# Kernel optimization log

Measured on AMD Instinct MI355X. Metric: run time of the kernel, lower is better.

Reference implementation:

```python
import jax, jax.numpy as jnp
import numpy as np

PH, PW = 7, 7          # pooled output size (fixed by offset shape in module)
SPP = 2                # sample_per_part: bilinear samples per bin edge
SS = 0.0625            # spatial_scale = 1/16
TRANS_STD = 0.1


def setup_inputs() -> dict:
    key = jax.random.key(0)
    k1, k2, k3, k4, k5 = jax.random.split(key, 5)
    B, C, H, W = 8, 256, 168, 168
    N = 512
    img = W / SS  # input-image extent = 2688
    features = jax.random.normal(k1, (B, C, H, W), dtype=jnp.float32)
    bidx = jax.random.randint(k2, (N,), 0, B).astype(jnp.float32)
    xs = jnp.sort(jax.random.uniform(k3, (N, 2), minval=0.0, maxval=img - 1.0), axis=1)
    ys = jnp.sort(jax.random.uniform(k4, (N, 2), minval=0.0, maxval=img - 1.0), axis=1)
    rois = jnp.stack([bidx, xs[:, 0], ys[:, 0],
                      jnp.minimum(xs[:, 1] + 16.0, img - 1.0),
                      jnp.minimum(ys[:, 1] + 16.0, img - 1.0)], axis=1)
    offset = jax.random.normal(k5, (N, 2, PH, PW), dtype=jnp.float32)
    return {"features": features, "rois": rois, "offset": offset}


def _deform_roi_pool(features, rois, offset):
    B, C, H, W = features.shape
    off = offset * TRANS_STD  # module scales offsets by trans_std
    bidx = jax.lax.stop_gradient(rois[:, 0]).astype(jnp.int32)
    x1, y1, x2, y2 = rois[:, 1], rois[:, 2], rois[:, 3], rois[:, 4]
    # DCN kernel ROI geometry (0.5-pixel aligned, min size 0.1)
    sw = x1 * SS - 0.5
    sh = y1 * SS - 0.5
    rw = jnp.maximum((x2 + 1.0) * SS - 0.5 - sw, 0.1)
    rh = jnp.maximum((y2 + 1.0) * SS - 0.5 - sh, 0.1)
    bin_w, bin_h = rw / PW, rh / PH
    sub_w, sub_h = bin_w / SPP, bin_h / SPP

    e5 = lambda v: v[:, None, None, None, None]  # [N] -> [N,1,1,1,1]
    pw = jnp.arange(PW, dtype=features.dtype).reshape(1, 1, PW, 1, 1)
    ph = jnp.arange(PH, dtype=features.dtype).reshape(1, PH, 1, 1, 1)
    iw = (jnp.arange(SPP, dtype=features.dtype) + 0.5).reshape(1, 1, 1, 1, SPP)
    ih = (jnp.arange(SPP, dtype=features.dtype) + 0.5).reshape(1, 1, 1, SPP, 1)
    offx = off[:, 0][:, :, :, None, None]  # [N,PH,PW,1,1]
    offy = off[:, 1][:, :, :, None, None]

    # sample coords [N,PH,PW,SPP,SPP]: bin start + per-bin learned shift + sub-sample
    x = e5(sw) + pw * e5(bin_w) + offx * e5(rw) + iw * e5(sub_w)
    y = e5(sh) + ph * e5(bin_h) + offy * e5(rh) + ih * e5(sub_h)

    valid = (x > -0.5) & (x < W - 0.5) & (y > -0.5) & (y < H - 0.5)
    xc = jnp.clip(x, 0.0, W - 1.0)
    yc = jnp.clip(y, 0.0, H - 1.0)
    x0f, y0f = jnp.floor(xc), jnp.floor(yc)
    lx, ly = xc - x0f, yc - y0f
    x0 = x0f.astype(jnp.int32)
    y0 = y0f.astype(jnp.int32)
    x1i = jnp.minimum(x0 + 1, W - 1)
    y1i = jnp.minimum(y0 + 1, H - 1)

    # flat gather over (batch, h, w), channels vectorized
    featf = jnp.transpose(features, (0, 2, 3, 1)).reshape(B * H * W, C)
    base = e5(bidx) * (H * W)
    g = lambda yy, xx: featf[base + yy * W + xx]  # [N,PH,PW,SPP,SPP,C]

    w00 = ((1 - ly) * (1 - lx))[..., None]
    w01 = ((1 - ly) * lx)[..., None]
    w10 = (ly * (1 - lx))[..., None]
    w11 = (ly * lx)[..., None]
    val = w00 * g(y0, x0) + w01 * g(y0, x1i) + w10 * g(y1i, x0) + w11 * g(y1i, x1i)
    val = jnp.where(valid[..., None], val, 0.0)

    s = val.sum(axis=(3, 4))                                   # [N,PH,PW,C]
    cnt = valid.sum(axis=(3, 4)).astype(features.dtype)[..., None]
    out = jnp.where(cnt > 0, s / jnp.maximum(cnt, 1.0), 0.0)
    return jnp.transpose(out, (0, 3, 1, 2))                    # [N,C,PH,PW]


def reference(features, rois, offset):
    return _deform_roi_pool(features, rois, offset)
```

## Files before the change

### kernel.cpp

```cpp
#include <hip/hip_runtime.h>
#include <hip/hip_fp16.h>


#define PH_ 7
#define PW_ 7
#define SPP_ 2
#define SS_ 0.0625f
#define TRANS_STD_ 0.1f
#define B_ 8
#define C_ 256
#define H_ 168
#define W_ 168
#define N_ 512
#define HW_ (H_ * W_)
#define HW4_ (HW_ / 4)
#define BLK_ 512
#define RPC_ 10

__global__ __launch_bounds__(512) void build_roi_lists(
    const float* __restrict__ rois, int* __restrict__ ws)
{
    const int r = threadIdx.x;
    if (r < B_) ws[r] = 0;
    __syncthreads();
    const int b = (int)rois[r * 5 + 0];
    const int pos = atomicAdd(&ws[b], 1);
    ws[B_ + b * N_ + pos] = r;
}

__global__ __launch_bounds__(BLK_) void droi_pool_lds(
    const float* __restrict__ features,
    const float* __restrict__ rois,
    const float* __restrict__ offset,
    float* __restrict__ out,
    const int* __restrict__ ws)
{
    __shared__ __half plane[HW_];

    const int c   = blockIdx.x;
    const int b   = blockIdx.y;
    const int tid = threadIdx.x;

    const float4* __restrict__ f4 =
        reinterpret_cast<const float4*>(features + (size_t)(b * C_ + c) * HW_);
    {
        const int full = HW4_ / BLK_;
#pragma unroll 4
        for (int k = 0; k < full; ++k) {
            const int i = tid + k * BLK_;
            const float4 v = f4[i];
            union { __half2 h[2]; float2 f2; } u;
            u.h[0].x = __float2half(v.x); u.h[0].y = __float2half(v.y);
            u.h[1].x = __float2half(v.z); u.h[1].y = __float2half(v.w);
            *reinterpret_cast<float2*>(&plane[i * 4]) = u.f2;
        }
        const int i = tid + full * BLK_;
        if (i < HW4_) {
            const float4 v = f4[i];
            union { __half2 h[2]; float2 f2; } u;
            u.h[0].x = __float2half(v.x); u.h[0].y = __float2half(v.y);
            u.h[1].x = __float2half(v.z); u.h[1].y = __float2half(v.w);
            *reinterpret_cast<float2*>(&plane[i * 4]) = u.f2;
        }
    }
    __syncthreads();

    const int cnt_b = ws[b];
    const int* __restrict__ list = ws + B_ + b * N_;

    const int q   = tid / 49;
    const int bin = tid - q * 49;
    const int ph  = bin / PW_;
    const int pw  = bin - ph * PW_;
    const bool lane_ok = (q < RPC_);

    for (int base = 0; base < cnt_b; base += RPC_) {
        const int idx     = base + q;
        const bool active = lane_ok && (idx < cnt_b);
        const int r = list[active ? idx : 0];

        const float x1r = rois[r * 5 + 1];
        const float y1r = rois[r * 5 + 2];
        const float x2r = rois[r * 5 + 3];
        const float y2r = rois[r * 5 + 4];

        const float sw    = x1r * SS_ - 0.5f;
        const float sh    = y1r * SS_ - 0.5f;
        const float rw    = fmaxf((x2r + 1.0f) * SS_ - 0.5f - sw, 0.1f);
        const float rh    = fmaxf((y2r + 1.0f) * SS_ - 0.5f - sh, 0.1f);
        const float bin_w = rw * (1.0f / PW_);
        const float bin_h = rh * (1.0f / PH_);
        const float sub_w = bin_w * (1.0f / SPP_);
        const float sub_h = bin_h * (1.0f / SPP_);

        const float offx = offset[((r * 2 + 0) * PH_ + ph) * PW_ + pw] * TRANS_STD_;
        const float offy = offset[((r * 2 + 1) * PH_ + ph) * PW_ + pw] * TRANS_STD_;

        const float bx = sw + (float)pw * bin_w + offx * rw;
        const float by = sh + (float)ph * bin_h + offy * rh;

        float s = 0.0f;
        int cnt = 0;
#pragma unroll
        for (int ihs = 0; ihs < SPP_; ++ihs) {
#pragma unroll
            for (int iws = 0; iws < SPP_; ++iws) {
                const float x = bx + ((float)iws + 0.5f) * sub_w;
                const float y = by + ((float)ihs + 0.5f) * sub_h;
                const bool valid = (x > -0.5f) && (x < (float)W_ - 0.5f) &&
                                   (y > -0.5f) && (y < (float)H_ - 0.5f);
                const float xc = fminf(fmaxf(x, 0.0f), (float)(W_ - 1));
                const float yc = fminf(fmaxf(y, 0.0f), (float)(H_ - 1));
                const float x0f = floorf(xc);
                const float y0f = floorf(yc);
                const float lx = xc - x0f;
                const float ly = yc - y0f;
                const int x0 = (int)x0f;
                const int y0 = (int)y0f;
                const int x1i = min(x0 + 1, W_ - 1);
                const int y1i = min(y0 + 1, H_ - 1);

                const float f00 = __half2float(plane[y0  * W_ + x0 ]);
                const float f01 = __half2float(plane[y0  * W_ + x1i]);
                const float f10 = __half2float(plane[y1i * W_ + x0 ]);
                const float f11 = __half2float(plane[y1i * W_ + x1i]);

                const float v = (1.0f - ly) * (1.0f - lx) * f00 +
                                (1.0f - ly) * lx          * f01 +
                                ly          * (1.0f - lx) * f10 +
                                ly          * lx          * f11;
                if (valid) { s += v; cnt += 1; }
            }
        }

        if (active) {
            const float res = (cnt > 0) ? (s / (float)cnt) : 0.0f;
            out[((size_t)r * C_ + c) * (PH_ * PW_) + bin] = res;
        }
    }
}

__global__ __launch_bounds__(64) void droi_pool_fallback(
    const float* __restrict__ features,
    const float* __restrict__ rois,
    const float* __restrict__ offset,
    float* __restrict__ out)
{
    const int blk  = blockIdx.x;
    const int n    = blk >> 8;
    const int c    = blk & 255;
    const int lane = threadIdx.x;
    if (lane >= PH_ * PW_) return;
    const int ph = lane / PW_;
    const int pw = lane % PW_;

    const float r0  = rois[n * 5 + 0];
    const float x1r = rois[n * 5 + 1];
    const float y1r = rois[n * 5 + 2];
    const float x2r = rois[n * 5 + 3];
    const float y2r = rois[n * 5 + 4];
    const int   b   = (int)r0;

    const float sw    = x1r * SS_ - 0.5f;
    const float sh    = y1r * SS_ - 0.5f;
    const float rw    = fmaxf((x2r + 1.0f) * SS_ - 0.5f - sw, 0.1f);
    const float rh    = fmaxf((y2r + 1.0f) * SS_ - 0.5f - sh, 0.1f);
    const float bin_w = rw / PW_;
    const float bin_h = rh / PH_;
    const float sub_w = bin_w / SPP_;
    const float sub_h = bin_h / SPP_;

    const float offx = offset[((n * 2 + 0) * PH_ + ph) * PW_ + pw] * TRANS_STD_;
    const float offy = offset[((n * 2 + 1) * PH_ + ph) * PW_ + pw] * TRANS_STD_;

    const float bx = sw + (float)pw * bin_w + offx * rw;
    const float by = sh + (float)ph * bin_h + offy * rh;

    const float* __restrict__ f =
        features + (size_t)(b * C_ + c) * (size_t)HW_;

    float s = 0.0f;
    int cnt = 0;
#pragma unroll
    for (int ihs = 0; ihs < SPP_; ++ihs) {
#pragma unroll
        for (int iws = 0; iws < SPP_; ++iws) {
            const float x = bx + ((float)iws + 0.5f) * sub_w;
            const float y = by + ((float)ihs + 0.5f) * sub_h;
            const bool valid = (x > -0.5f) && (x < (float)W_ - 0.5f) &&
                               (y > -0.5f) && (y < (float)H_ - 0.5f);
            const float xc = fminf(fmaxf(x, 0.0f), (float)(W_ - 1));
            const float yc = fminf(fmaxf(y, 0.0f), (float)(H_ - 1));
            const float x0f = floorf(xc);
            const float y0f = floorf(yc);
            const float lx = xc - x0f;
            const float ly = yc - y0f;
            const int x0 = (int)x0f;
            const int y0 = (int)y0f;
            const int x1i = min(x0 + 1, W_ - 1);
            const int y1i = min(y0 + 1, H_ - 1);
            const float f00 = f[y0  * W_ + x0 ];
            const float f01 = f[y0  * W_ + x1i];
            const float f10 = f[y1i * W_ + x0 ];
            const float f11 = f[y1i * W_ + x1i];
            const float v = (1.0f - ly) * (1.0f - lx) * f00 +
                            (1.0f - ly) * lx          * f01 +
                            ly          * (1.0f - lx) * f10 +
                            ly          * lx          * f11;
            if (valid) { s += v; cnt += 1; }
        }
    }
    const float res = (cnt > 0) ? (s / (float)cnt) : 0.0f;
    out[(size_t)(n * C_ + c) * (PH_ * PW_) + lane] = res;
}

extern "C" void kernel_launch(void* const* d_in, const int* in_sizes, int n_in,
                              void* d_out, int out_size, void* d_ws, size_t ws_size,
                              hipStream_t stream) {
    const float* features = (const float*)d_in[0];
    const float* rois     = (const float*)d_in[1];
    const float* offset   = (const float*)d_in[2];
    float*       out      = (float*)d_out;

    const size_t ws_needed = (size_t)(B_ + B_ * N_) * sizeof(int);
    if (ws_size >= ws_needed) {
        int* ws = (int*)d_ws;
        hipLaunchKernelGGL(build_roi_lists, dim3(1), dim3(N_), 0, stream,
                           rois, ws);
        hipLaunchKernelGGL(droi_pool_lds, dim3(C_, B_), dim3(BLK_), 0, stream,
                           features, rois, offset, out, ws);
    } else {
        hipLaunchKernelGGL(droi_pool_fallback, dim3(N_ * C_), dim3(64), 0, stream,
                           features, rois, offset, out);
    }
}
```

Before: 357.4 us.

## Precompute per-ROI sample descriptors and enlarge pooling blocks to 1024 threads

Adds a kernel that computes, once per ROI, bin and sub-sample each packed corner address, interpolation fractions and a validity-scaled weight. This removes the per-channel repetition of the geometry math in the pooling kernel, which now only reads a float4 descriptor and does the interpolation with lerps. The pooling block grows to 1024 threads and handles 20 ROIs per iteration. The trade-off is an extra kernel launch, a larger workspace requirement (about 1.6 MB of descriptors read by every block) and a larger block that may affect occupancy.

```diff
diff --git a/kernel.cpp b/kernel.cpp
--- a/kernel.cpp
+++ b/kernel.cpp
@@ -14,8 +14,15 @@
 #define N_ 512
 #define HW_ (H_ * W_)
 #define HW4_ (HW_ / 4)
-#define BLK_ 512
-#define RPC_ 10
+#define BINS_ (PH_ * PW_)
+#define NSUB_ (SPP_ * SPP_)
+#define BLK_ 1024
+#define RPC_ 20
+
+#define WS_LIST_OFF_  B_
+#define WS_DESC_OFF_I (B_ + B_ * N_)
+#define DESC_FLOATS_  (N_ * NSUB_ * BINS_ * 4)
+#define WS_NEEDED_    ((size_t)(WS_DESC_OFF_I) * 4 + (size_t)DESC_FLOATS_ * 4)
 
 __global__ __launch_bounds__(512) void build_roi_lists(
     const float* __restrict__ rois, int* __restrict__ ws)
@@ -25,13 +32,81 @@
     __syncthreads();
     const int b = (int)rois[r * 5 + 0];
     const int pos = atomicAdd(&ws[b], 1);
-    ws[B_ + b * N_ + pos] = r;
-}
-
-__global__ __launch_bounds__(BLK_) void droi_pool_lds(
-    const float* __restrict__ features,
+    ws[WS_LIST_OFF_ + b * N_ + pos] = r;
+}
+
+__global__ __launch_bounds__(64) void build_desc(
     const float* __restrict__ rois,
     const float* __restrict__ offset,
+    float4* __restrict__ desc)
+{
+    const int r   = blockIdx.x;
+    const int bin = threadIdx.x;
+    if (bin >= BINS_) return;
+    const int ph = bin / PW_;
+    const int pw = bin - ph * PW_;
+
+    const float x1r = rois[r * 5 + 1];
+    const float y1r = rois[r * 5 + 2];
+    const float x2r = rois[r * 5 + 3];
+    const float y2r = rois[r * 5 + 4];
+
+    const float sw    = x1r * SS_ - 0.5f;
+    const float sh    = y1r * SS_ - 0.5f;
+    const float rw    = fmaxf((x2r + 1.0f) * SS_ - 0.5f - sw, 0.1f);
+    const float rh    = fmaxf((y2r + 1.0f) * SS_ - 0.5f - sh, 0.1f);
+    const float bin_w = rw * (1.0f / PW_);
+    const float bin_h = rh * (1.0f / PH_);
+    const float sub_w = bin_w * (1.0f / SPP_);
+    const float sub_h = bin_h * (1.0f / SPP_);
+
+    const float offx = offset[((r * 2 + 0) * PH_ + ph) * PW_ + pw] * TRANS_STD_;
+    const float offy = offset[((r * 2 + 1) * PH_ + ph) * PW_ + pw] * TRANS_STD_;
+
+    const float bx = sw + (float)pw * bin_w + offx * rw;
+    const float by = sh + (float)ph * bin_h + offy * rh;
+
+    unsigned pack[NSUB_];
+    float lxs[NSUB_], lys[NSUB_];
+    int   vals[NSUB_];
+    int   cnt = 0;
+#pragma unroll
+    for (int s = 0; s < NSUB_; ++s) {
+        const int ihs = s >> 1;
+        const int iws = s & 1;
+        const float x = bx + ((float)iws + 0.5f) * sub_w;
+        const float y = by + ((float)ihs + 0.5f) * sub_h;
+        const int valid = (x > -0.5f) && (x < (float)W_ - 0.5f) &&
+                          (y > -0.5f) && (y < (float)H_ - 0.5f);
+        const float xc = fminf(fmaxf(x, 0.0f), (float)(W_ - 1));
+        const float yc = fminf(fmaxf(y, 0.0f), (float)(H_ - 1));
+        const float x0f = floorf(xc);
+        const float y0f = floorf(yc);
+        const int x0 = (int)x0f;
+        const int y0 = (int)y0f;
+        const int dx = (x0 + 1 <= W_ - 1) ? 1 : 0;
+        const int dy = (y0 + 1 <= H_ - 1) ? 1 : 0;
+        pack[s] = (unsigned)(y0 * W_ + x0) | ((unsigned)dx << 15) |
+                  ((unsigned)dy << 16);
+        lxs[s] = xc - x0f;
+        lys[s] = yc - y0f;
+        vals[s] = valid;
+        cnt += valid;
+    }
+    const float inv = (cnt > 0) ? (1.0f / (float)cnt) : 0.0f;
+#pragma unroll
+    for (int s = 0; s < NSUB_; ++s) {
+        float4 d;
+        d.x = __uint_as_float(pack[s]);
+        d.y = lxs[s];
+        d.z = lys[s];
+        d.w = vals[s] ? inv : 0.0f;
+        desc[((size_t)r * NSUB_ + s) * BINS_ + bin] = d;
+    }
+}
+
+__global__ __launch_bounds__(BLK_, 8) void droi_pool_lds(
+    const float* __restrict__ features,
     float* __restrict__ out,
     const int* __restrict__ ws)
 {
@@ -43,35 +118,22 @@
 
     const float4* __restrict__ f4 =
         reinterpret_cast<const float4*>(features + (size_t)(b * C_ + c) * HW_);
-    {
-        const int full = HW4_ / BLK_;
-#pragma unroll 4
-        for (int k = 0; k < full; ++k) {
-            const int i = tid + k * BLK_;
-            const float4 v = f4[i];
-            union { __half2 h[2]; float2 f2; } u;
-            u.h[0].x = __float2half(v.x); u.h[0].y = __float2half(v.y);
-            u.h[1].x = __float2half(v.z); u.h[1].y = __float2half(v.w);
-            *reinterpret_cast<float2*>(&plane[i * 4]) = u.f2;
-        }
-        const int i = tid + full * BLK_;
-        if (i < HW4_) {
-            const float4 v = f4[i];
-            union { __half2 h[2]; float2 f2; } u;
-            u.h[0].x = __float2half(v.x); u.h[0].y = __float2half(v.y);
-            u.h[1].x = __float2half(v.z); u.h[1].y = __float2half(v.w);
-            *reinterpret_cast<float2*>(&plane[i * 4]) = u.f2;
-        }
+    for (int i = tid; i < HW4_; i += BLK_) {
+        const float4 v = f4[i];
+        union { __half2 h[2]; float2 f2; } u;
+        u.h[0].x = __float2half(v.x); u.h[0].y = __float2half(v.y);
+        u.h[1].x = __float2half(v.z); u.h[1].y = __float2half(v.w);
+        *reinterpret_cast<float2*>(&plane[i * 4]) = u.f2;
     }
     __syncthreads();
 
     const int cnt_b = ws[b];
-    const int* __restrict__ list = ws + B_ + b * N_;
-
-    const int q   = tid / 49;
-    const int bin = tid - q * 49;
-    const int ph  = bin / PW_;
-    const int pw  = bin - ph * PW_;
+    const int* __restrict__ list = ws + WS_LIST_OFF_ + b * N_;
+    const float4* __restrict__ desc =
+        reinterpret_cast<const float4*>(ws + WS_DESC_OFF_I);
+
+    const int q   = tid / BINS_;
+    const int bin = tid - q * BINS_;
     const bool lane_ok = (q < RPC_);
 
     for (int base = 0; base < cnt_b; base += RPC_) {
@@ -79,63 +141,29 @@
         const bool active = lane_ok && (idx < cnt_b);
         const int r = list[active ? idx : 0];
 
-        const float x1r = rois[r * 5 + 1];
-        const float y1r = rois[r * 5 + 2];
-        const float x2r = rois[r * 5 + 3];
-        const float y2r = rois[r * 5 + 4];
-
-        const float sw    = x1r * SS_ - 0.5f;
-        const float sh    = y1r * SS_ - 0.5f;
-        const float rw    = fmaxf((x2r + 1.0f) * SS_ - 0.5f - sw, 0.1f);
-        const float rh    = fmaxf((y2r + 1.0f) * SS_ - 0.5f - sh, 0.1f);
-        const float bin_w = rw * (1.0f / PW_);
-        const float bin_h = rh * (1.0f / PH_);
-        const float sub_w = bin_w * (1.0f / SPP_);
-        const float sub_h = bin_h * (1.0f / SPP_);
-
-        const float offx = offset[((r * 2 + 0) * PH_ + ph) * PW_ + pw] * TRANS_STD_;
-        const float offy = offset[((r * 2 + 1) * PH_ + ph) * PW_ + pw] * TRANS_STD_;
-
-        const float bx = sw + (float)pw * bin_w + offx * rw;
-        const float by = sh + (float)ph * bin_h + offy * rh;
-
-        float s = 0.0f;
-        int cnt = 0;
-#pragma unroll
-        for (int ihs = 0; ihs < SPP_; ++ihs) {
-#pragma unroll
-            for (int iws = 0; iws < SPP_; ++iws) {
-                const float x = bx + ((float)iws + 0.5f) * sub_w;
-                const float y = by + ((float)ihs + 0.5f) * sub_h;
-                const bool valid = (x > -0.5f) && (x < (float)W_ - 0.5f) &&
-                                   (y > -0.5f) && (y < (float)H_ - 0.5f);
-                const float xc = fminf(fmaxf(x, 0.0f), (float)(W_ - 1));
-                const float yc = fminf(fmaxf(y, 0.0f), (float)(H_ - 1));
-                const float x0f = floorf(xc);
-                const float y0f = floorf(yc);
-                const float lx = xc - x0f;
-                const float ly = yc - y0f;
-                const int x0 = (int)x0f;
-                const int y0 = (int)y0f;
-                const int x1i = min(x0 + 1, W_ - 1);
-                const int y1i = min(y0 + 1, H_ - 1);
-
-                const float f00 = __half2float(plane[y0  * W_ + x0 ]);
-                const float f01 = __half2float(plane[y0  * W_ + x1i]);
-                const float f10 = __half2float(plane[y1i * W_ + x0 ]);
-                const float f11 = __half2float(plane[y1i * W_ + x1i]);
-
-                const float v = (1.0f - ly) * (1.0f - lx) * f00 +
-                                (1.0f - ly) * lx          * f01 +
-                                ly          * (1.0f - lx) * f10 +
-                                ly          * lx          * f11;
-                if (valid) { s += v; cnt += 1; }
-            }
+        float acc = 0.0f;
+#pragma unroll
+        for (int s = 0; s < NSUB_; ++s) {
+            const float4 d = desc[((size_t)r * NSUB_ + s) * BINS_ + bin];
+            const unsigned pk = __float_as_uint(d.x);
+            const int a00 = (int)(pk & 0x7FFFu);
+            const int dx  = (int)((pk >> 15) & 1u);
+            const int a10 = a00 + (int)((pk >> 16) & 1u) * W_;
+            const float lx = d.y;
+            const float ly = d.z;
+
+            const float f00 = __half2float(plane[a00]);
+            const float f01 = __half2float(plane[a00 + dx]);
+            const float f10 = __half2float(plane[a10]);
+            const float f11 = __half2float(plane[a10 + dx]);
+
+            const float top = f00 + lx * (f01 - f00);
+            const float bot = f10 + lx * (f11 - f10);
+            acc += d.w * (top + ly * (bot - top));
         }
 
         if (active) {
-            const float res = (cnt > 0) ? (s / (float)cnt) : 0.0f;
-            out[((size_t)r * C_ + c) * (PH_ * PW_) + bin] = res;
+            out[((size_t)r * C_ + c) * BINS_ + bin] = acc;
         }
     }
 }
@@ -150,7 +178,7 @@
     const int n    = blk >> 8;
     const int c    = blk & 255;
     const int lane = threadIdx.x;
-    if (lane >= PH_ * PW_) return;
+    if (lane >= BINS_) return;
     const int ph = lane / PW_;
     const int pw = lane % PW_;
 
@@ -211,7 +239,7 @@
         }
     }
     const float res = (cnt > 0) ? (s / (float)cnt) : 0.0f;
-    out[(size_t)(n * C_ + c) * (PH_ * PW_) + lane] = res;
+    out[(size_t)(n * C_ + c) * BINS_ + lane] = res;
 }
 
 extern "C" void kernel_launch(void* const* d_in, const int* in_sizes, int n_in,
@@ -222,13 +250,15 @@
     const float* offset   = (const float*)d_in[2];
     float*       out      = (float*)d_out;
 
-    const size_t ws_needed = (size_t)(B_ + B_ * N_) * sizeof(int);
-    if (ws_size >= ws_needed) {
+    if (ws_size >= WS_NEEDED_) {
         int* ws = (int*)d_ws;
+        float4* desc = reinterpret_cast<float4*>(ws + WS_DESC_OFF_I);
         hipLaunchKernelGGL(build_roi_lists, dim3(1), dim3(N_), 0, stream,
                            rois, ws);
+        hipLaunchKernelGGL(build_desc, dim3(N_), dim3(64), 0, stream,
+                           rois, offset, desc);
         hipLaunchKernelGGL(droi_pool_lds, dim3(C_, B_), dim3(BLK_), 0, stream,
-                           features, rois, offset, out, ws);
+                           features, out, ws);
     } else {
         hipLaunchKernelGGL(droi_pool_fallback, dim3(N_ * C_), dim3(64), 0, stream,
                            features, rois, offset, out);
```

Measured after the change: 346.0 us. -3.2%, faster.
